# Kernel tuning notes

Measured on AMD Instinct MI355X. Metric: run time of the kernel, lower is better.

The kernel has to match this reference:

```python
import jax, jax.numpy as jnp
import numpy as np

B, S, D, H = 4, 2048, 1024, 16
HD = D // H
DFF = 4 * D
EPS = 1e-5


def gelu_tanh(x):
    c = jnp.sqrt(jnp.asarray(2.0 / jnp.pi, x.dtype))
    return 0.5 * x * (1.0 + jnp.tanh(c * (x + 0.044715 * x ** 3)))


def layernorm(x, scale, shift):
    mean = jnp.mean(x, axis=-1, keepdims=True)
    var = jnp.var(x, axis=-1, keepdims=True)  # unbiased=False
    return scale * (x - mean) * jax.lax.rsqrt(var + EPS) + shift


def setup_inputs() -> dict:
    key = jax.random.key(0)
    ks = jax.random.split(key, 12)
    s_in = 1.0 / np.sqrt(D)
    s_ff = 1.0 / np.sqrt(DFF)
    return {
        "x": jax.random.normal(ks[0], (B, S, D), jnp.float32),
        "Wq": jax.random.uniform(ks[1], (D, D), jnp.float32, -s_in, s_in),
        "Wk": jax.random.uniform(ks[2], (D, D), jnp.float32, -s_in, s_in),
        "Wv": jax.random.uniform(ks[3], (D, D), jnp.float32, -s_in, s_in),
        "Wo": jax.random.uniform(ks[4], (D, D), jnp.float32, -s_in, s_in),
        "bo": jax.random.uniform(ks[5], (D,), jnp.float32, -s_in, s_in),
        "W1": jax.random.uniform(ks[6], (D, DFF), jnp.float32, -s_in, s_in),
        "b1": jax.random.uniform(ks[7], (DFF,), jnp.float32, -s_in, s_in),
        "W2": jax.random.uniform(ks[8], (DFF, D), jnp.float32, -s_ff, s_ff),
        "b2": jax.random.uniform(ks[9], (D,), jnp.float32, -s_ff, s_ff),
        "ln1_scale": jnp.ones((D,), jnp.float32),
        "ln1_shift": jnp.zeros((D,), jnp.float32),
        "ln2_scale": jnp.ones((D,), jnp.float32),
        "ln2_shift": jnp.zeros((D,), jnp.float32),
    }


def reference(x, Wq, Wk, Wv, Wo, bo, W1, b1, W2, b2,
              ln1_scale, ln1_shift, ln2_scale, ln2_shift):
    # --- pre-LN causal MHA ---
    h = layernorm(x, ln1_scale, ln1_shift)
    q = (h @ Wq).reshape(B, S, H, HD).transpose(0, 2, 1, 3)  # [B,H,S,hd]
    k = (h @ Wk).reshape(B, S, H, HD).transpose(0, 2, 1, 3)
    v = (h @ Wv).reshape(B, S, H, HD).transpose(0, 2, 1, 3)
    scores = jnp.einsum('bhqd,bhkd->bhqk', q, k)
    causal = jnp.tril(jnp.ones((S, S), bool))  # mask strict upper triangle
    scores = jnp.where(causal, scores, -jnp.inf)
    attn = jax.nn.softmax(scores / np.sqrt(HD), axis=-1)
    ctx = jnp.einsum('bhqk,bhkd->bhqd', attn, v)
    ctx = ctx.transpose(0, 2, 1, 3).reshape(B, S, D)
    x = x + (ctx @ Wo + bo)
    # --- FFN ---
    h = layernorm(x, ln2_scale, ln2_shift)
    h = gelu_tanh(h @ W1 + b1) @ W2 + b2
    return x + h
```

## Files before the change

### kernel.cpp

```cpp
#include <hip/hip_runtime.h>
#include <math.h>

#define S_LEN  2048
#define DMODEL 1024
#define NHEAD  16
#define BATCH  4
#define NROWS  (BATCH*S_LEN)
#define DFF    4096
#define QKV_LD 3072

typedef __attribute__((ext_vector_type(4))) unsigned short us4;
typedef __attribute__((ext_vector_type(8))) unsigned short us8;
typedef __attribute__((ext_vector_type(8))) __bf16 bf16x8;
typedef __attribute__((ext_vector_type(4))) float f32x4;

#if __has_builtin(__builtin_amdgcn_exp2f)
#define EXP2(x) __builtin_amdgcn_exp2f(x)
#else
#define EXP2(x) exp2f(x)
#endif
#if __has_builtin(__builtin_amdgcn_rcpf)
#define RCP(x) __builtin_amdgcn_rcpf(x)
#else
#define RCP(x) (1.0f/(x))
#endif

static __device__ __forceinline__ unsigned short f2bf(float f) {
  __bf16 b = (__bf16)f;
  return __builtin_bit_cast(unsigned short, b);
}
#define GLD16(gp, lp) __builtin_amdgcn_global_load_lds( \
    (const __attribute__((address_space(1))) unsigned int*)(gp), \
    (__attribute__((address_space(3))) unsigned int*)(lp), 16, 0, 0)

static __device__ __forceinline__ int xcd_swz(int bid, int nwg) {
  int q = nwg >> 3;
  return (bid & 7) * q + (bid >> 3);
}

__global__ __launch_bounds__(256) void ln_kernel(
    const float* __restrict__ x, const float* __restrict__ scale,
    const float* __restrict__ shift, unsigned short* __restrict__ out)
{
  const int row = blockIdx.x, tid = threadIdx.x;
  const int lane = tid & 63, wave = tid >> 6;
  const float* xr = x + (size_t)row * DMODEL;
  f32x4 v = *(const f32x4*)&xr[tid * 4];
  float s  = v[0]+v[1]+v[2]+v[3];
  float s2 = v[0]*v[0]+v[1]*v[1]+v[2]*v[2]+v[3]*v[3];
  #pragma unroll
  for (int m = 1; m < 64; m <<= 1) { s += __shfl_xor(s, m); s2 += __shfl_xor(s2, m); }
  __shared__ float red[8];
  if (lane == 0) { red[wave] = s; red[4 + wave] = s2; }
  __syncthreads();
  s  = red[0]+red[1]+red[2]+red[3];
  s2 = red[4]+red[5]+red[6]+red[7];
  float mean = s * (1.0f/DMODEL);
  float var  = s2 * (1.0f/DMODEL) - mean*mean;
  float rstd = rsqrtf(var + 1e-5f);
  us4 o;
  #pragma unroll
  for (int j = 0; j < 4; j++) {
    float val = (v[j]-mean)*rstd*scale[tid*4+j] + shift[tid*4+j];
    o[j] = f2bf(val);
  }
  *(us4*)&out[(size_t)row*DMODEL + tid*4] = o;
}

__global__ __launch_bounds__(256) void wtrans_all(
    const float* __restrict__ Wq, const float* __restrict__ Wk,
    const float* __restrict__ Wv, const float* __restrict__ Wo,
    const float* __restrict__ W1, const float* __restrict__ W2,
    unsigned short* __restrict__ wqkvt, unsigned short* __restrict__ wot,
    unsigned short* __restrict__ w1t, unsigned short* __restrict__ w2t,
    float sclq)
{
  __shared__ unsigned short tile[64][72];
  const int bid = blockIdx.x, tid = threadIdx.x;
  const float* W; unsigned short* Wt; int K, N, sub; float scl = 1.0f;
  if (bid < 1024) {
    int wsel = bid >> 8; sub = bid & 255; K = 1024; N = 1024;
    W  = (wsel == 0) ? Wq : (wsel == 1) ? Wk : (wsel == 2) ? Wv : Wo;
    Wt = (wsel == 0) ? wqkvt : (wsel == 1) ? wqkvt + 1024*1024
       : (wsel == 2) ? wqkvt + 2048*1024 : wot;
    if (wsel == 0) scl = sclq;
  } else if (bid < 2048) { sub = bid - 1024; K = 1024; N = 4096; W = W1; Wt = w1t; }
  else                   { sub = bid - 2048; K = 4096; N = 1024; W = W2; Wt = w2t; }
  const int nbn = N >> 6;
  const int kt = sub / nbn, nt = sub % nbn;
  int r = tid >> 2, c0 = (tid & 3) << 4;
  const float* src = W + (size_t)(kt*64 + r)*N + nt*64 + c0;
  #pragma unroll
  for (int j = 0; j < 16; j += 4) {
    f32x4 f = *(const f32x4*)&src[j];
    tile[r][c0+j+0] = f2bf(f[0]*scl); tile[r][c0+j+1] = f2bf(f[1]*scl);
    tile[r][c0+j+2] = f2bf(f[2]*scl); tile[r][c0+j+3] = f2bf(f[3]*scl);
  }
  __syncthreads();
  int n = tid >> 2, k0 = (tid & 3) << 4;
  us8 o0, o1;
  #pragma unroll
  for (int j = 0; j < 8; j++) { o0[j] = tile[k0+j][n]; o1[j] = tile[k0+8+j][n]; }
  unsigned short* dst = Wt + (size_t)(nt*64 + n)*K + kt*64 + k0;
  *(us8*)&dst[0] = o0;
  *(us8*)&dst[8] = o1;
}

__global__ __launch_bounds__(256) void vtrans(
    const unsigned short* __restrict__ v, unsigned short* __restrict__ vt)
{
  __shared__ unsigned short tile[64][72];
  const int tid = threadIdx.x;
  const int bh = blockIdx.x >> 5, st = blockIdx.x & 31;
  const int b = bh >> 4, h = bh & 15;
  int r = tid >> 2, c0 = (tid & 3) << 4;
  const unsigned short* src = v + (size_t)(b*S_LEN + st*64 + r)*QKV_LD + h*64 + c0;
  *(us8*)&tile[r][c0]   = *(const us8*)&src[0];
  *(us8*)&tile[r][c0+8] = *(const us8*)&src[8];
  __syncthreads();
  int d = tid >> 2, s0 = (tid & 3) << 4;
  us8 o0, o1;
  #pragma unroll
  for (int j = 0; j < 8; j++) { o0[j] = tile[s0+j][d]; o1[j] = tile[s0+8+j][d]; }
  unsigned short* dst = vt + (size_t)(bh*64 + d)*S_LEN + st*64 + s0;
  *(us8*)&dst[0] = o0;
  *(us8*)&dst[8] = o1;
}

template<bool BIAS, bool GELU_>
__global__ __launch_bounds__(512, 2) void gemm256(
    const unsigned short* __restrict__ A, const unsigned short* __restrict__ Bt,
    unsigned short* __restrict__ Cout, const float* __restrict__ bias,
    int M, int N, int K)
{
  constexpr int BN = 256, WN = 64, NF = 4;
  __shared__ unsigned short sA[2][256*64];
  __shared__ unsigned short sB[2][BN*64];
  const int tid = threadIdx.x;
  const int wave = tid >> 6, lane = tid & 63;
  const int wm = wave >> 2, wn = wave & 3;
  const int l15 = lane & 15, g = lane >> 4, x7 = lane & 7, r8 = lane >> 3;
  const int srcc = (x7 ^ r8) << 3;
  const int nbn = N / BN;
  const int bid = xcd_swz(blockIdx.x, gridDim.x);
  const int bm = bid / nbn, bn = bid % nbn;
  const unsigned short* gA = A  + (size_t)(bm*256)*K;
  const unsigned short* gB = Bt + (size_t)(bn*BN)*K;
  const int NT = K >> 6;

  f32x4 acc[8][NF] = {};

#define STAGEA(buf, h, kb) do { \
    _Pragma("unroll") \
    for (int j_ = 0; j_ < 2; j_++) \
      GLD16(gA + (size_t)((h)*128 + j_*64 + wave*8 + r8)*K + (kb) + srcc, \
            &sA[buf][((h)*128 + j_*64 + wave*8)*64]); \
  } while (0)
#define STAGEB(buf, h, kb) do { \
    _Pragma("unroll") \
    for (int j_ = 0; j_ < 2; j_++) \
      GLD16(gB + (size_t)((h)*128 + j_*64 + wave*8 + r8)*K + (kb) + srcc, \
            &sB[buf][((h)*128 + j_*64 + wave*8)*64]); \
  } while (0)
#define RDA_(m, kk) (*(const bf16x8*)&cA[(wm*128 + (m)*16 + l15)*64 + ((((kk)*4+g)^x7)<<3)])
#define RDB_(n, kk) (*(const bf16x8*)&cB[(wn*WN + (n)*16 + l15)*64 + ((((kk)*4+g)^x7)<<3)])
#define PH(p) do { \
    __builtin_amdgcn_s_setprio(1); \
    _Pragma("unroll") for (int mm_ = 0; mm_ < 2; mm_++) \
    _Pragma("unroll") for (int n_ = 0; n_ < NF; n_++) \
    _Pragma("unroll") for (int kk_ = 0; kk_ < 2; kk_++) \
      acc[(p)*2+mm_][n_] = __builtin_amdgcn_mfma_f32_16x16x32_bf16( \
          af[mm_][kk_], bfr[n_][kk_], acc[(p)*2+mm_][n_], 0, 0, 0); \
    __builtin_amdgcn_s_setprio(0); \
  } while (0)

  STAGEB(0, 0, 0); STAGEB(0, 1, 0);
  STAGEA(0, 0, 0); STAGEA(0, 1, 0);
  STAGEB(1, 0, 64); STAGEB(1, 1, 64);

  for (int t = 0; t < NT; ++t) {
    const int c = t & 1;
    const unsigned short* cA = sA[c];
    const unsigned short* cB = sB[c];
    const int kb1 = (t + 1) * 64, kb2 = (t + 2) * 64;
    bf16x8 af[2][2], bfr[NF][2];

    if (t < NT - 1) asm volatile("s_waitcnt vmcnt(4)" ::: "memory");
    else            asm volatile("s_waitcnt vmcnt(0)" ::: "memory");
    __builtin_amdgcn_s_barrier();
    __builtin_amdgcn_sched_barrier(0);

    #pragma unroll
    for (int n = 0; n < NF; n++) { bfr[n][0] = RDB_(n, 0); bfr[n][1] = RDB_(n, 1); }
    af[0][0] = RDA_(0, 0); af[0][1] = RDA_(0, 1);
    af[1][0] = RDA_(1, 0); af[1][1] = RDA_(1, 1);
    if (t + 1 < NT) STAGEA(c ^ 1, 0, kb1);
    PH(0);
    af[0][0] = RDA_(2, 0); af[0][1] = RDA_(2, 1);
    af[1][0] = RDA_(3, 0); af[1][1] = RDA_(3, 1);
    if (t + 1 < NT) STAGEA(c ^ 1, 1, kb1);
    PH(1);
    __builtin_amdgcn_s_barrier();
    af[0][0] = RDA_(4, 0); af[0][1] = RDA_(4, 1);
    af[1][0] = RDA_(5, 0); af[1][1] = RDA_(5, 1);
    if (t + 2 < NT) STAGEB(c, 0, kb2);
    PH(2);
    af[0][0] = RDA_(6, 0); af[0][1] = RDA_(6, 1);
    af[1][0] = RDA_(7, 0); af[1][1] = RDA_(7, 1);
    if (t + 2 < NT) STAGEB(c, 1, kb2);
    PH(3);
  }

  #pragma unroll
  for (int m = 0; m < 8; m++) {
    #pragma unroll
    for (int r = 0; r < 4; r++) {
      int grow = bm*256 + wm*128 + m*16 + g*4 + r;
      #pragma unroll
      for (int n = 0; n < NF; n++) {
        int gcol = bn*BN + wn*WN + n*16 + l15;
        float v = acc[m][n][r];
        if (BIAS) v += bias[gcol];
        if (GELU_) {
          float xx = v;
          float u = 0.7978845608f*(xx + 0.044715f*xx*xx*xx);
          float e = EXP2(u * 2.88539008f);
          float th = 1.0f - 2.0f*RCP(e + 1.0f);
          v = 0.5f*xx*(1.0f + th);
        }
        Cout[(size_t)grow*N + gcol] = f2bf(v);
      }
    }
  }
#undef STAGEA
#undef STAGEB
#undef RDA_
#undef RDB_
#undef PH
}

template<bool BIAS, bool GELU_, bool RESID, bool OUTF32>
__global__ __launch_bounds__(512, 2) void gemm128(
    const unsigned short* __restrict__ A, const unsigned short* __restrict__ Bt,
    void* Cout, const float* __restrict__ bias, const float* resid,
    int M, int N, int K)
{
  __shared__ unsigned short sA[2][128*64];
  __shared__ unsigned short sB[2][256*64];
  const int tid = threadIdx.x;
  const int wave = tid >> 6, lane = tid & 63;
  const int wm = wave >> 2, wn = wave & 3;
  const int l15 = lane & 15, g = lane >> 4, x7 = lane & 7, r8 = lane >> 3;
  const int srcc = (x7 ^ r8) << 3;
  const int nbn = N >> 8;
  const int bid = xcd_swz(blockIdx.x, gridDim.x);
  const int bm = bid / nbn, bn = bid % nbn;
  const unsigned short* gA = A  + (size_t)(bm*128)*K;
  const unsigned short* gB = Bt + (size_t)(bn*256)*K;
  const int NT = K >> 6;

  f32x4 acc[4][4] = {};

#define STAGEA1(buf, kb) do { \
    _Pragma("unroll") \
    for (int j_ = 0; j_ < 2; j_++) \
      GLD16(gA + (size_t)(j_*64 + wave*8 + r8)*K + (kb) + srcc, \
            &sA[buf][(j_*64 + wave*8)*64]); \
  } while (0)
#define STAGEB1(buf, kb) do { \
    _Pragma("unroll") \
    for (int j_ = 0; j_ < 4; j_++) \
      GLD16(gB + (size_t)(j_*64 + wave*8 + r8)*K + (kb) + srcc, \
            &sB[buf][(j_*64 + wave*8)*64]); \
  } while (0)
#define RDA1(m, kk) (*(const bf16x8*)&cA[(wm*64 + (m)*16 + l15)*64 + ((((kk)*4+g)^x7)<<3)])
#define RDB1(n, kk) (*(const bf16x8*)&cB[(wn*64 + (n)*16 + l15)*64 + ((((kk)*4+g)^x7)<<3)])
#define PH1(p) do { \
    __builtin_amdgcn_s_setprio(1); \
    _Pragma("unroll") for (int mm_ = 0; mm_ < 2; mm_++) \
    _Pragma("unroll") for (int n_ = 0; n_ < 4; n_++) \
    _Pragma("unroll") for (int kk_ = 0; kk_ < 2; kk_++) \
      acc[(p)*2+mm_][n_] = __builtin_amdgcn_mfma_f32_16x16x32_bf16( \
          af[mm_][kk_], bfr[n_][kk_], acc[(p)*2+mm_][n_], 0, 0, 0); \
    __builtin_amdgcn_s_setprio(0); \
  } while (0)

  STAGEB1(0, 0);
  STAGEA1(0, 0);
  STAGEB1(1, 64);

  for (int t = 0; t < NT; ++t) {
    const int c = t & 1;
    const unsigned short* cA = sA[c];
    const unsigned short* cB = sB[c];
    const int kb1 = (t + 1) * 64, kb2 = (t + 2) * 64;
    bf16x8 af[2][2], bfr[4][2];

    if (t < NT - 1) asm volatile("s_waitcnt vmcnt(4)" ::: "memory");
    else            asm volatile("s_waitcnt vmcnt(0)" ::: "memory");
    __builtin_amdgcn_s_barrier();
    __builtin_amdgcn_sched_barrier(0);

    #pragma unroll
    for (int n = 0; n < 4; n++) { bfr[n][0] = RDB1(n, 0); bfr[n][1] = RDB1(n, 1); }
    af[0][0] = RDA1(0, 0); af[0][1] = RDA1(0, 1);
    af[1][0] = RDA1(1, 0); af[1][1] = RDA1(1, 1);
    if (t + 1 < NT) STAGEA1(c ^ 1, kb1);
    PH1(0);
    __builtin_amdgcn_s_barrier();
    af[0][0] = RDA1(2, 0); af[0][1] = RDA1(2, 1);
    af[1][0] = RDA1(3, 0); af[1][1] = RDA1(3, 1);
    if (t + 2 < NT) STAGEB1(c, kb2);
    PH1(1);
  }

  #pragma unroll
  for (int m = 0; m < 4; m++) {
    #pragma unroll
    for (int r = 0; r < 4; r++) {
      int grow = bm*128 + wm*64 + m*16 + g*4 + r;
      #pragma unroll
      for (int n = 0; n < 4; n++) {
        int gcol = bn*256 + wn*64 + n*16 + l15;
        float v = acc[m][n][r];
        if (BIAS) v += bias[gcol];
        if (GELU_) {
          float xx = v;
          float u = 0.7978845608f*(xx + 0.044715f*xx*xx*xx);
          float e = EXP2(u * 2.88539008f);
          float th = 1.0f - 2.0f*RCP(e + 1.0f);
          v = 0.5f*xx*(1.0f + th);
        }
        if (RESID) v += resid[(size_t)grow*N + gcol];
        if (OUTF32) ((float*)Cout)[(size_t)grow*N + gcol] = v;
        else ((unsigned short*)Cout)[(size_t)grow*N + gcol] = f2bf(v);
      }
    }
  }
#undef STAGEA1
#undef STAGEB1
#undef RDA1
#undef RDB1
#undef PH1
}

__global__ __launch_bounds__(512) void attn_kernel(
    const unsigned short* __restrict__ qb, const unsigned short* __restrict__ kb,
    const unsigned short* __restrict__ vt, unsigned short* __restrict__ ctx)
{
  __shared__ unsigned short sK[2][64*64];
  __shared__ unsigned short sV[2][64*64];
  __shared__ unsigned short sP[8][16*64];
  const int tid = threadIdx.x, wave = tid >> 6, lane = tid & 63;
  const int l15 = lane & 15, g = lane >> 4, x7 = lane & 7;
  const int qt = 15 - (blockIdx.x >> 6);
  const int bh = blockIdx.x & 63;
  const int b = bh >> 4, h = bh & 15;
  const int qrow = qt*128 + wave*16;
  const int NTI = 2*qt + 2;

  bf16x8 qf[2];
  {
    const unsigned short* qr = qb + (size_t)(b*S_LEN + qrow + l15) * QKV_LD + h*64;
    qf[0] = *(const bf16x8*)&qr[g*8];
    qf[1] = *(const bf16x8*)&qr[32 + g*8];
  }

  us8 ones_u;
  #pragma unroll
  for (int j = 0; j < 8; j++) ones_u[j] = 0x3F80;
  const bf16x8 ones8 = __builtin_bit_cast(bf16x8, ones_u);

  f32x4 oacc[4] = {};
  f32x4 lacc = {};
  float mrow[4];
  #pragma unroll
  for (int r = 0; r < 4; r++) mrow[r] = -INFINITY;

  const int rrow = lane >> 3;
  const int srcc = (x7 ^ rrow) << 3;
  const unsigned short* kbase = kb + (size_t)(b*S_LEN)*QKV_LD + h*64 + srcc;
  const unsigned short* vbase = vt + (size_t)(bh*64)*S_LEN + srcc;

#define ASTAGE(buf, t) do { \
    const int kv0_ = (t)*64; \
    GLD16(kbase + (size_t)(kv0_ + wave*8 + rrow)*QKV_LD, &sK[buf][wave*8*64]); \
    GLD16(vbase + (size_t)(wave*8 + rrow)*S_LEN + kv0_,  &sV[buf][wave*8*64]); \
  } while(0)

  ASTAGE(0, 0);

  for (int t = 0; t < NTI; ++t) {
    __syncthreads();
    const int cur = t & 1;
    if (t < NTI - 1) ASTAGE(cur ^ 1, t + 1);

    const int kv0 = t*64;
    if (kv0 > qrow + 15) continue;

    f32x4 sacc[4] = {};
    __builtin_amdgcn_s_setprio(1);
    #pragma unroll
    for (int kk = 0; kk < 2; kk++) {
      const int csw = ((kk*4 + g) ^ x7) << 3;
      #pragma unroll
      for (int n = 0; n < 4; n++) {
        bf16x8 kf = *(const bf16x8*)&sK[cur][(n*16 + l15)*64 + csw];
        sacc[n] = __builtin_amdgcn_mfma_f32_16x16x32_bf16(qf[kk], kf, sacc[n], 0, 0, 0);
      }
    }
    __builtin_amdgcn_s_setprio(0);

    float p[4][4], rm[4];
    const bool masked = (kv0 + 63 > qrow);
    #pragma unroll
    for (int r = 0; r < 4; r++) {
      float m_ = -INFINITY;
      #pragma unroll
      for (int n = 0; n < 4; n++) {
        float sc = sacc[n][r];
        if (masked && (kv0 + n*16 + l15) > (qrow + g*4 + r)) sc = -INFINITY;
        p[n][r] = sc;
        m_ = fmaxf(m_, sc);
      }
      rm[r] = m_;
    }
    bool need = (rm[0] > mrow[0] + 8.0f) | (rm[1] > mrow[1] + 8.0f) |
                (rm[2] > mrow[2] + 8.0f) | (rm[3] > mrow[3] + 8.0f);
    if (__any(need)) {
      #pragma unroll
      for (int r = 0; r < 4; r++) {
        float vv = rm[r];
        vv = fmaxf(vv, __shfl_xor(vv, 1));
        vv = fmaxf(vv, __shfl_xor(vv, 2));
        vv = fmaxf(vv, __shfl_xor(vv, 4));
        vv = fmaxf(vv, __shfl_xor(vv, 8));
        float mn = fmaxf(mrow[r], vv);
        float alpha = EXP2(mrow[r] - mn);
        mrow[r] = mn;
        lacc[r] *= alpha;
        #pragma unroll
        for (int nd = 0; nd < 4; nd++) oacc[nd][r] *= alpha;
      }
    }
    #pragma unroll
    for (int n = 0; n < 4; n++)
      #pragma unroll
      for (int r = 0; r < 4; r++)
        p[n][r] = EXP2(p[n][r] - mrow[r]);

    #pragma unroll
    for (int n = 0; n < 4; n++) {
      const int chunk = n*2 + (l15 >> 3);
      #pragma unroll
      for (int r = 0; r < 4; r++) {
        const int prow = g*4 + r;
        sP[wave][prow*64 + ((chunk ^ (prow & 7)) << 3) + x7] = f2bf(p[n][r]);
      }
    }
    asm volatile("s_waitcnt lgkmcnt(0)" ::: "memory");
    __builtin_amdgcn_sched_barrier(0);

    __builtin_amdgcn_s_setprio(1);
    #pragma unroll
    for (int kk = 0; kk < 2; kk++) {
      const int csw = ((kk*4 + g) ^ x7) << 3;
      bf16x8 pa = *(const bf16x8*)&sP[wave][l15*64 + csw];
      #pragma unroll
      for (int nd = 0; nd < 4; nd++) {
        bf16x8 vf = *(const bf16x8*)&sV[cur][(nd*16 + l15)*64 + csw];
        oacc[nd] = __builtin_amdgcn_mfma_f32_16x16x32_bf16(pa, vf, oacc[nd], 0, 0, 0);
      }
      lacc = __builtin_amdgcn_mfma_f32_16x16x32_bf16(pa, ones8, lacc, 0, 0, 0);
    }
    __builtin_amdgcn_s_setprio(0);
  }

  #pragma unroll
  for (int r = 0; r < 4; r++) {
    float inv = RCP(lacc[r]);
    size_t row = (size_t)(b*S_LEN + qrow + g*4 + r);
    #pragma unroll
    for (int nd = 0; nd < 4; nd++)
      ctx[row*DMODEL + h*64 + nd*16 + l15] = f2bf(oacc[nd][r] * inv);
  }
}

extern "C" void kernel_launch(void* const* d_in, const int* in_sizes, int n_in,
                              void* d_out, int out_size, void* d_ws, size_t ws_size,
                              hipStream_t stream)
{
  const float* x    = (const float*)d_in[0];
  const float* Wq   = (const float*)d_in[1];
  const float* Wk   = (const float*)d_in[2];
  const float* Wv   = (const float*)d_in[3];
  const float* Wo   = (const float*)d_in[4];
  const float* bo   = (const float*)d_in[5];
  const float* W1   = (const float*)d_in[6];
  const float* b1   = (const float*)d_in[7];
  const float* W2   = (const float*)d_in[8];
  const float* b2   = (const float*)d_in[9];
  const float* ln1s = (const float*)d_in[10];
  const float* ln1b = (const float*)d_in[11];
  const float* ln2s = (const float*)d_in[12];
  const float* ln2b = (const float*)d_in[13];
  float* out = (float*)d_out;
  (void)in_sizes; (void)n_in; (void)out_size; (void)ws_size;

  char* ws = (char*)d_ws;
  size_t off = 0;
  auto alloc = [&](size_t n) { char* p = ws + off; off += (n + 255) & ~(size_t)255; return p; };
  unsigned short* hbuf  = (unsigned short*)alloc((size_t)NROWS*DMODEL*2);
  unsigned short* qkv   = (unsigned short*)alloc((size_t)NROWS*QKV_LD*2);
  unsigned short* vtb   = (unsigned short*)alloc((size_t)NROWS*DMODEL*2);
  unsigned short* ctx   = (unsigned short*)alloc((size_t)NROWS*DMODEL*2);
  unsigned short* ffn1  = (unsigned short*)alloc((size_t)NROWS*DFF*2);
  unsigned short* wqkvt = (unsigned short*)alloc((size_t)QKV_LD*DMODEL*2);
  unsigned short* wot   = (unsigned short*)alloc((size_t)DMODEL*DMODEL*2);
  unsigned short* w1t   = (unsigned short*)alloc((size_t)DFF*DMODEL*2);
  unsigned short* w2t   = (unsigned short*)alloc((size_t)DMODEL*DFF*2);

  const float SCLQ = 0.18033688011f;

  wtrans_all<<<dim3(3072), dim3(256), 0, stream>>>(
      Wq, Wk, Wv, Wo, W1, W2, wqkvt, wot, w1t, w2t, SCLQ);

  ln_kernel<<<dim3(NROWS), dim3(256), 0, stream>>>(x, ln1s, ln1b, hbuf);
  gemm256<false,false><<<dim3(32*12), dim3(512), 0, stream>>>(
      hbuf, wqkvt, qkv, nullptr, NROWS, QKV_LD, DMODEL);
  vtrans<<<dim3(2048), dim3(256), 0, stream>>>(qkv + 2048, vtb);
  attn_kernel<<<dim3(1024), dim3(512), 0, stream>>>(qkv, qkv + 1024, vtb, ctx);
  gemm128<true,false,true,true><<<dim3(64*4), dim3(512), 0, stream>>>(
      ctx, wot, (void*)out, bo, x, NROWS, DMODEL, DMODEL);
  ln_kernel<<<dim3(NROWS), dim3(256), 0, stream>>>(out, ln2s, ln2b, hbuf);
  gemm256<true,true><<<dim3(32*16), dim3(512), 0, stream>>>(
      hbuf, w1t, ffn1, b1, NROWS, DFF, DMODEL);
  gemm128<true,false,true,true><<<dim3(64*4), dim3(512), 0, stream>>>(
      ffn1, w2t, (void*)out, b2, out, NROWS, DMODEL, DFF);
}
```

Measured before the change: 357.5 us.

## Double attention query tile per block to reuse staged K/V tiles

Each attention block now covers 256 query rows instead of 128, with every wave handling two 16-row query groups that share each K/V tile staged in LDS. This halves the grid and the global K/V loads per query row, cutting memory traffic and barrier overhead per unit of work. In exchange each wave holds twice the accumulators and Q fragments, which raises register pressure, and with 512 blocks of uneven causal length the load balance across CUs may get worse. An extra LDS wait is added before the P write, since the sP buffer is now reused within the same tile.

Measured after the change: 381.4 us. 6.7% more time.

```diff
diff --git a/kernel.cpp b/kernel.cpp
--- a/kernel.cpp
+++ b/kernel.cpp
@@ -353,17 +353,18 @@
   __shared__ unsigned short sP[8][16*64];
   const int tid = threadIdx.x, wave = tid >> 6, lane = tid & 63;
   const int l15 = lane & 15, g = lane >> 4, x7 = lane & 7;
-  const int qt = 15 - (blockIdx.x >> 6);
+  const int qt = 7 - (blockIdx.x >> 6);
   const int bh = blockIdx.x & 63;
   const int b = bh >> 4, h = bh & 15;
-  const int qrow = qt*128 + wave*16;
-  const int NTI = 2*qt + 2;
-
-  bf16x8 qf[2];
-  {
-    const unsigned short* qr = qb + (size_t)(b*S_LEN + qrow + l15) * QKV_LD + h*64;
-    qf[0] = *(const bf16x8*)&qr[g*8];
-    qf[1] = *(const bf16x8*)&qr[32 + g*8];
+  const int qrow0 = qt*256 + wave*32;
+  const int NTI = 4*qt + 4;
+
+  bf16x8 qf[2][2];
+  #pragma unroll
+  for (int gq = 0; gq < 2; gq++) {
+    const unsigned short* qr = qb + (size_t)(b*S_LEN + qrow0 + gq*16 + l15) * QKV_LD + h*64;
+    qf[gq][0] = *(const bf16x8*)&qr[g*8];
+    qf[gq][1] = *(const bf16x8*)&qr[32 + g*8];
   }
 
   us8 ones_u;
@@ -371,11 +372,13 @@
   for (int j = 0; j < 8; j++) ones_u[j] = 0x3F80;
   const bf16x8 ones8 = __builtin_bit_cast(bf16x8, ones_u);
 
-  f32x4 oacc[4] = {};
-  f32x4 lacc = {};
-  float mrow[4];
-  #pragma unroll
-  for (int r = 0; r < 4; r++) mrow[r] = -INFINITY;
+  f32x4 oacc[2][4] = {};
+  f32x4 lacc[2] = {};
+  float mrow[2][4];
+  #pragma unroll
+  for (int gq = 0; gq < 2; gq++)
+    #pragma unroll
+    for (int r = 0; r < 4; r++) mrow[gq][r] = -INFINITY;
 
   const int rrow = lane >> 3;
   const int srcc = (x7 ^ rrow) << 3;
@@ -396,94 +399,104 @@
     if (t < NTI - 1) ASTAGE(cur ^ 1, t + 1);
 
     const int kv0 = t*64;
-    if (kv0 > qrow + 15) continue;
-
-    f32x4 sacc[4] = {};
-    __builtin_amdgcn_s_setprio(1);
-    #pragma unroll
-    for (int kk = 0; kk < 2; kk++) {
-      const int csw = ((kk*4 + g) ^ x7) << 3;
+    if (kv0 > qrow0 + 31) continue;
+
+    #pragma unroll
+    for (int gq = 0; gq < 2; gq++) {
+      const int qrowg = qrow0 + gq*16;
+      if (kv0 > qrowg + 15) continue;
+
+      f32x4 sacc[4] = {};
+      __builtin_amdgcn_s_setprio(1);
+      #pragma unroll
+      for (int kk = 0; kk < 2; kk++) {
+        const int csw = ((kk*4 + g) ^ x7) << 3;
+        #pragma unroll
+        for (int n = 0; n < 4; n++) {
+          bf16x8 kf = *(const bf16x8*)&sK[cur][(n*16 + l15)*64 + csw];
+          sacc[n] = __builtin_amdgcn_mfma_f32_16x16x32_bf16(qf[gq][kk], kf, sacc[n], 0, 0, 0);
+        }
+      }
+      __builtin_amdgcn_s_setprio(0);
+
+      float p[4][4], rm[4];
+      const bool masked = (kv0 + 63 > qrowg);
+      #pragma unroll
+      for (int r = 0; r < 4; r++) {
+        float m_ = -INFINITY;
+        #pragma unroll
+        for (int n = 0; n < 4; n++) {
+          float sc = sacc[n][r];
+          if (masked && (kv0 + n*16 + l15) > (qrowg + g*4 + r)) sc = -INFINITY;
+          p[n][r] = sc;
+          m_ = fmaxf(m_, sc);
+        }
+        rm[r] = m_;
+      }
+      bool need = (rm[0] > mrow[gq][0] + 8.0f) | (rm[1] > mrow[gq][1] + 8.0f) |
+                  (rm[2] > mrow[gq][2] + 8.0f) | (rm[3] > mrow[gq][3] + 8.0f);
+      if (__any(need)) {
+        #pragma unroll
+        for (int r = 0; r < 4; r++) {
+          float vv = rm[r];
+          vv = fmaxf(vv, __shfl_xor(vv, 1));
+          vv = fmaxf(vv, __shfl_xor(vv, 2));
+          vv = fmaxf(vv, __shfl_xor(vv, 4));
+          vv = fmaxf(vv, __shfl_xor(vv, 8));
+          float mn = fmaxf(mrow[gq][r], vv);
+          float alpha = EXP2(mrow[gq][r] - mn);
+          mrow[gq][r] = mn;
+          lacc[gq][r] *= alpha;
+          #pragma unroll
+          for (int nd = 0; nd < 4; nd++) oacc[gq][nd][r] *= alpha;
+        }
+      }
+      #pragma unroll
+      for (int n = 0; n < 4; n++)
+        #pragma unroll
+        for (int r = 0; r < 4; r++)
+          p[n][r] = EXP2(p[n][r] - mrow[gq][r]);
+
+      asm volatile("s_waitcnt lgkmcnt(0)" ::: "memory");
+      __builtin_amdgcn_sched_barrier(0);
       #pragma unroll
       for (int n = 0; n < 4; n++) {
-        bf16x8 kf = *(const bf16x8*)&sK[cur][(n*16 + l15)*64 + csw];
-        sacc[n] = __builtin_amdgcn_mfma_f32_16x16x32_bf16(qf[kk], kf, sacc[n], 0, 0, 0);
-      }
+        const int chunk = n*2 + (l15 >> 3);
+        #pragma unroll
+        for (int r = 0; r < 4; r++) {
+          const int prow = g*4 + r;
+          sP[wave][prow*64 + ((chunk ^ (prow & 7)) << 3) + x7] = f2bf(p[n][r]);
+        }
+      }
+      asm volatile("s_waitcnt lgkmcnt(0)" ::: "memory");
+      __builtin_amdgcn_sched_barrier(0);
+
+      __builtin_amdgcn_s_setprio(1);
+      #pragma unroll
+      for (int kk = 0; kk < 2; kk++) {
+        const int csw = ((kk*4 + g) ^ x7) << 3;
+        bf16x8 pa = *(const bf16x8*)&sP[wave][l15*64 + csw];
+        #pragma unroll
+        for (int nd = 0; nd < 4; nd++) {
+          bf16x8 vf = *(const bf16x8*)&sV[cur][(nd*16 + l15)*64 + csw];
+          oacc[gq][nd] = __builtin_amdgcn_mfma_f32_16x16x32_bf16(pa, vf, oacc[gq][nd], 0, 0, 0);
+        }
+        lacc[gq] = __builtin_amdgcn_mfma_f32_16x16x32_bf16(pa, ones8, lacc[gq], 0, 0, 0);
+      }
+      __builtin_amdgcn_s_setprio(0);
     }
-    __builtin_amdgcn_s_setprio(0);
-
-    float p[4][4], rm[4];
-    const bool masked = (kv0 + 63 > qrow);
+  }
+
+  #pragma unroll
+  for (int gq = 0; gq < 2; gq++)
     #pragma unroll
     for (int r = 0; r < 4; r++) {
-      float m_ = -INFINITY;
-      #pragma unroll
-      for (int n = 0; n < 4; n++) {
-        float sc = sacc[n][r];
-        if (masked && (kv0 + n*16 + l15) > (qrow + g*4 + r)) sc = -INFINITY;
-        p[n][r] = sc;
-        m_ = fmaxf(m_, sc);
-      }
-      rm[r] = m_;
+      float inv = RCP(lacc[gq][r]);
+      size_t row = (size_t)(b*S_LEN + qrow0 + gq*16 + g*4 + r);
+      #pragma unroll
+      for (int nd = 0; nd < 4; nd++)
+        ctx[row*DMODEL + h*64 + nd*16 + l15] = f2bf(oacc[gq][nd][r] * inv);
     }
-    bool need = (rm[0] > mrow[0] + 8.0f) | (rm[1] > mrow[1] + 8.0f) |
-                (rm[2] > mrow[2] + 8.0f) | (rm[3] > mrow[3] + 8.0f);
-    if (__any(need)) {
-      #pragma unroll
-      for (int r = 0; r < 4; r++) {
-        float vv = rm[r];
-        vv = fmaxf(vv, __shfl_xor(vv, 1));
-        vv = fmaxf(vv, __shfl_xor(vv, 2));
-        vv = fmaxf(vv, __shfl_xor(vv, 4));
-        vv = fmaxf(vv, __shfl_xor(vv, 8));
-        float mn = fmaxf(mrow[r], vv);
-        float alpha = EXP2(mrow[r] - mn);
-        mrow[r] = mn;
-        lacc[r] *= alpha;
-        #pragma unroll
-        for (int nd = 0; nd < 4; nd++) oacc[nd][r] *= alpha;
-      }
-    }
-    #pragma unroll
-    for (int n = 0; n < 4; n++)
-      #pragma unroll
-      for (int r = 0; r < 4; r++)
-        p[n][r] = EXP2(p[n][r] - mrow[r]);
-
-    #pragma unroll
-    for (int n = 0; n < 4; n++) {
-      const int chunk = n*2 + (l15 >> 3);
-      #pragma unroll
-      for (int r = 0; r < 4; r++) {
-        const int prow = g*4 + r;
-        sP[wave][prow*64 + ((chunk ^ (prow & 7)) << 3) + x7] = f2bf(p[n][r]);
-      }
-    }
-    asm volatile("s_waitcnt lgkmcnt(0)" ::: "memory");
-    __builtin_amdgcn_sched_barrier(0);
-
-    __builtin_amdgcn_s_setprio(1);
-    #pragma unroll
-    for (int kk = 0; kk < 2; kk++) {
-      const int csw = ((kk*4 + g) ^ x7) << 3;
-      bf16x8 pa = *(const bf16x8*)&sP[wave][l15*64 + csw];
-      #pragma unroll
-      for (int nd = 0; nd < 4; nd++) {
-        bf16x8 vf = *(const bf16x8*)&sV[cur][(nd*16 + l15)*64 + csw];
-        oacc[nd] = __builtin_amdgcn_mfma_f32_16x16x32_bf16(pa, vf, oacc[nd], 0, 0, 0);
-      }
-      lacc = __builtin_amdgcn_mfma_f32_16x16x32_bf16(pa, ones8, lacc, 0, 0, 0);
-    }
-    __builtin_amdgcn_s_setprio(0);
-  }
-
-  #pragma unroll
-  for (int r = 0; r < 4; r++) {
-    float inv = RCP(lacc[r]);
-    size_t row = (size_t)(b*S_LEN + qrow + g*4 + r);
-    #pragma unroll
-    for (int nd = 0; nd < 4; nd++)
-      ctx[row*DMODEL + h*64 + nd*16 + l15] = f2bf(oacc[nd][r] * inv);
-  }
 }
 
 extern "C" void kernel_launch(void* const* d_in, const int* in_sizes, int n_in,
@@ -529,7 +542,7 @@
   gemm256<false,false><<<dim3(32*12), dim3(512), 0, stream>>>(
       hbuf, wqkvt, qkv, nullptr, NROWS, QKV_LD, DMODEL);
   vtrans<<<dim3(2048), dim3(256), 0, stream>>>(qkv + 2048, vtb);
-  attn_kernel<<<dim3(1024), dim3(512), 0, stream>>>(qkv, qkv + 1024, vtb, ctx);
+  attn_kernel<<<dim3(512), dim3(512), 0, stream>>>(qkv, qkv + 1024, vtb, ctx);
   gemm128<true,false,true,true><<<dim3(64*4), dim3(512), 0, stream>>>(
       ctx, wot, (void*)out, bo, x, NROWS, DMODEL, DMODEL);
   ln_kernel<<<dim3(NROWS), dim3(256), 0, stream>>>(out, ln2s, ln2b, hbuf);
```
